# Kernel tuning notes

Measured on AMD Instinct MI355X. Metric: run time of the kernel, lower is better.

Reference implementation:

```python
import jax, jax.numpy as jnp
import numpy as np

N_LEVELS = 16
N_FEATS = 2
LOG2_T = 19
BASE_RES = 16.0
FINEST_RES = 512.0
N_POINTS = 1_000_000
HASH_MASK = np.uint32((1 << LOG2_T) - 1)
PRIME1 = np.uint32(2654435761)  # second spatial-hash prime (first is 1)


def setup_inputs() -> dict:
    key = jax.random.key(0)
    k1, k2 = jax.random.split(key)
    x = jax.random.uniform(k1, (N_POINTS, 2), dtype=jnp.float32)
    # nn.init.uniform_(w, -1e-4, 1e-4) per level, stacked: [L, T, F]
    embeddings = (jax.random.uniform(k2, (N_LEVELS, 2 ** LOG2_T, N_FEATS), dtype=jnp.float32) * 2.0 - 1.0) * 1e-4
    return {"x": x, "embeddings": embeddings}


def reference(x, embeddings):
    L = N_LEVELS
    n = x.shape[0]
    # per-level resolutions: floor(base * b**i)
    b = np.exp((np.log(FINEST_RES) - np.log(BASE_RES)) / (L - 1))
    res = np.floor(BASE_RES * b ** np.arange(L)).astype(np.float32)  # [L]
    res_j = jnp.asarray(res)

    pixels = x[None, :, :] * res_j[:, None, None]           # [L, n, 2]
    top_left = jnp.floor(pixels).astype(jnp.int32)          # [L, n, 2]
    offsets = jnp.array([[0, 0], [1, 0], [0, 1], [1, 1]], dtype=jnp.int32)
    box = top_left[:, :, None, :] + offsets[None, None]     # [L, n, 4, 2]
    box = jnp.clip(box, 0, res_j[:, None, None, None].astype(jnp.int32))

    # spatial hash: (c0*1 ^ c1*prime) & mask, with uint32 wraparound like torch int32
    c = box.astype(jnp.uint32)
    addr = ((c[..., 0] * np.uint32(1)) ^ (c[..., 1] * PRIME1)) & HASH_MASK  # [L, n, 4]
    addr = addr.astype(jnp.int32)

    # gather per-level corner features: [L, n, 4, F]
    feats = jax.vmap(lambda table, idx: table[idx])(embeddings, addr)

    # bilinear interpolation
    w = pixels - jnp.floor(pixels)                          # [L, n, 2]
    w0 = w[..., 0:1]
    w1 = w[..., 1:2]
    f0, f1, f2, f3 = feats[:, :, 0], feats[:, :, 1], feats[:, :, 2], feats[:, :, 3]
    f = (f0 * (1 - w0) + f1 * w0) * (1 - w1) + (f2 * (1 - w0) + f3 * w0) * w1  # [L, n, F]

    # concat levels along feature dim -> [n, L*F]
    return jnp.transpose(f, (1, 0, 2)).reshape(n, L * N_FEATS)
```

## Files before the change

kernel.cpp:

```cpp
#include <hip/hip_runtime.h>
#include <cmath>

#define NLVL 16
#define TSIZE (1u << 19)
#define HMASK ((1u << 19) - 1u)
#define PRIME1 2654435761u

struct Params {
    float rf[NLVL];
    int   ri[NLVL];
    int   base[NLVL];
    int   stride[NLVL];
};

__global__ __launch_bounds__(256) void build_dense(
    const float2* __restrict__ emb, float2* __restrict__ dense, Params p)
{
    const int l = blockIdx.y;
    const int cy = blockIdx.x;
    const int ri = p.ri[l];
    if (cy > ri) return;
    const unsigned hy = (unsigned)cy * PRIME1;
    const float2* tab = emb + (size_t)l * TSIZE;
    float2* drow = dense + p.base[l] + (size_t)cy * p.stride[l];
    for (int cx = threadIdx.x; cx <= ri; cx += 256)
        drow[cx] = tab[((unsigned)cx ^ hy) & HMASK];
}

__global__ __launch_bounds__(256) void hash_embed_dense(
    const float2* __restrict__ x,
    const float2* __restrict__ dense,
    float* __restrict__ out,
    Params p, int n)
{
    __shared__ float2 lds[NLVL * 256];
    const int tid = threadIdx.x;
    const int i = blockIdx.x * 256 + tid;
    float2 xy = make_float2(0.f, 0.f);
    if (i < n) xy = x[i];

    #pragma unroll
    for (int half = 0; half < 2; ++half) {
        float4 r0[8], r1[8];
        float w0v[8], w1v[8];
        int edge[8];
        #pragma unroll
        for (int j = 0; j < 8; ++j) {
            const int l = half * 8 + j;
            const float rf = p.rf[l];
            const int ri = p.ri[l];
            const float px = xy.x * rf, py = xy.y * rf;
            const float fx = floorf(px), fy = floorf(py);
            w0v[j] = px - fx;
            w1v[j] = py - fy;
            const int tx = (int)fx, ty = (int)fy;
            const int cx0 = min(tx, ri);
            const int cy0 = min(ty, ri);
            const int cy1 = min(ty + 1, ri);
            edge[j] = (cx0 == ri);
            const float2* tab = dense + p.base[l];
            const float2* a0 = tab + cy0 * p.stride[l] + cx0;
            const float2* a1 = tab + cy1 * p.stride[l] + cx0;
            __builtin_memcpy(&r0[j], a0, 16);
            __builtin_memcpy(&r1[j], a1, 16);
        }
        #pragma unroll
        for (int j = 0; j < 8; ++j) {
            const int l = half * 8 + j;
            const float w0 = w0v[j], w1 = w1v[j];
            const float u0 = 1.f - w0, u1 = 1.f - w1;
            const float e00x = r0[j].x, e00y = r0[j].y;
            const float e01x = edge[j] ? r0[j].x : r0[j].z;
            const float e01y = edge[j] ? r0[j].y : r0[j].w;
            const float e10x = r1[j].x, e10y = r1[j].y;
            const float e11x = edge[j] ? r1[j].x : r1[j].z;
            const float e11y = edge[j] ? r1[j].y : r1[j].w;
            const float g0 = (e00x*u0 + e01x*w0)*u1 + (e10x*u0 + e11x*w0)*w1;
            const float g1 = (e00y*u0 + e01y*w0)*u1 + (e10y*u0 + e11y*w0)*w1;
            lds[l * 256 + tid] = make_float2(g0, g1);
        }
    }
    __syncthreads();

    const float* lf = (const float*)lds;
    const long long total = (long long)n * 32;
    const long long base = (long long)blockIdx.x * 8192;
    #pragma unroll
    for (int it = 0; it < 8; ++it) {
        const int k = (it * 256 + tid) * 4;
        if (base + k < total) {
            const int p2 = k >> 5;
            const int l0 = (k & 31) >> 1;
            float4 v;
            v.x = lf[(l0 * 256 + p2) * 2 + 0];
            v.y = lf[(l0 * 256 + p2) * 2 + 1];
            v.z = lf[((l0 + 1) * 256 + p2) * 2 + 0];
            v.w = lf[((l0 + 1) * 256 + p2) * 2 + 1];
            *(float4*)(out + base + k) = v;
        }
    }
}

__global__ __launch_bounds__(256) void hash_embed_direct(
    const float2* __restrict__ x,
    const float2* __restrict__ emb,
    float* __restrict__ out,
    Params p, int n)
{
    __shared__ float2 lds[NLVL * 256];
    const int tid = threadIdx.x;
    const int i = blockIdx.x * 256 + tid;
    float2 xy = make_float2(0.f, 0.f);
    if (i < n) xy = x[i];

    #pragma unroll
    for (int half = 0; half < 2; ++half) {
        float2 f[32];
        float w0v[8], w1v[8];
        #pragma unroll
        for (int j = 0; j < 8; ++j) {
            const int l = half * 8 + j;
            const float rf = p.rf[l];
            const int ri = p.ri[l];
            const float px = xy.x * rf, py = xy.y * rf;
            const float fx = floorf(px), fy = floorf(py);
            w0v[j] = px - fx;
            w1v[j] = py - fy;
            const int tx = (int)fx, ty = (int)fy;
            const unsigned cx0 = (unsigned)min(tx, ri);
            const unsigned cy0 = (unsigned)min(ty, ri);
            const unsigned cx1 = (unsigned)min(tx + 1, ri);
            const unsigned cy1 = (unsigned)min(ty + 1, ri);
            const unsigned hy0 = cy0 * PRIME1;
            const unsigned hy1 = cy1 * PRIME1;
            const float2* tab = emb + (size_t)l * TSIZE;
            f[j*4+0] = tab[(cx0 ^ hy0) & HMASK];
            f[j*4+1] = tab[(cx1 ^ hy0) & HMASK];
            f[j*4+2] = tab[(cx0 ^ hy1) & HMASK];
            f[j*4+3] = tab[(cx1 ^ hy1) & HMASK];
        }
        #pragma unroll
        for (int j = 0; j < 8; ++j) {
            const int l = half * 8 + j;
            const float w0 = w0v[j], w1 = w1v[j];
            const float u0 = 1.f - w0, u1 = 1.f - w1;
            const float2 f0 = f[j*4+0], f1 = f[j*4+1], f2 = f[j*4+2], f3 = f[j*4+3];
            const float g0 = (f0.x*u0 + f1.x*w0)*u1 + (f2.x*u0 + f3.x*w0)*w1;
            const float g1 = (f0.y*u0 + f1.y*w0)*u1 + (f2.y*u0 + f3.y*w0)*w1;
            lds[l * 256 + tid] = make_float2(g0, g1);
        }
    }
    __syncthreads();

    const float* lf = (const float*)lds;
    const long long total = (long long)n * 32;
    const long long base = (long long)blockIdx.x * 8192;
    #pragma unroll
    for (int it = 0; it < 8; ++it) {
        const int k = (it * 256 + tid) * 4;
        if (base + k < total) {
            const int p2 = k >> 5;
            const int l0 = (k & 31) >> 1;
            float4 v;
            v.x = lf[(l0 * 256 + p2) * 2 + 0];
            v.y = lf[(l0 * 256 + p2) * 2 + 1];
            v.z = lf[((l0 + 1) * 256 + p2) * 2 + 0];
            v.w = lf[((l0 + 1) * 256 + p2) * 2 + 1];
            *(float4*)(out + base + k) = v;
        }
    }
}

extern "C" void kernel_launch(void* const* d_in, const int* in_sizes, int n_in,
                              void* d_out, int out_size, void* d_ws, size_t ws_size,
                              hipStream_t stream) {
    const float2* x = (const float2*)d_in[0];
    const float2* emb = (const float2*)d_in[1];
    float* out = (float*)d_out;
    const int n = in_sizes[0] / 2;

    Params p;
    int off = 0;
    const double b = std::exp((std::log(512.0) - std::log(16.0)) / 15.0);
    for (int l = 0; l < NLVL; ++l) {
        const double r = std::floor(16.0 * std::pow(b, (double)l));
        p.rf[l] = (float)r;
        p.ri[l] = (int)r;
        p.stride[l] = p.ri[l] + 2;
        p.base[l] = off;
        off += (p.ri[l] + 1) * (p.ri[l] + 2);
    }
    const size_t need = (size_t)off * sizeof(float2);

    const int grid = (n + 255) / 256;
    if (ws_size >= need) {
        build_dense<<<dim3(513, 16), 256, 0, stream>>>(emb, (float2*)d_ws, p);
        hash_embed_dense<<<grid, 256, 0, stream>>>(x, (const float2*)d_ws, out, p, n);
    } else {
        hash_embed_direct<<<grid, 256, 0, stream>>>(x, emb, out, p, n);
    }
}
```

Measured before the change: 281.4 us.

## Store dense embedding grid as scaled fp16 pairs and use nontemporal stores

The dense per-level grid is now built with each float2 embedding quantized to two fp16 values packed in 32 bits, scaled by 1024 to avoid subnormals. It is then dequantized in the lookup kernel. This halves the workspace size and gather bytes, aiming to cut memory traffic and improve cache hit rates. The change also swizzles the LDS layout and uses nontemporal loads and stores for the streaming table read and the output write. The trade-off is reduced precision of the embedding values, which may affect tolerance.

```diff
diff --git a/kernel.cpp b/kernel.cpp
--- a/kernel.cpp
+++ b/kernel.cpp
@@ -1,10 +1,17 @@
 #include <hip/hip_runtime.h>
+#include <hip/hip_fp16.h>
 #include <cmath>
 
 #define NLVL 16
 #define TSIZE (1u << 19)
 #define HMASK ((1u << 19) - 1u)
 #define PRIME1 2654435761u
+#define FSCALE 1024.0f
+#define FINV   (1.0f/1024.0f)
+
+typedef float f32x4 __attribute__((ext_vector_type(4)));
+typedef unsigned int       u32;
+typedef unsigned long long u64;
 
 struct Params {
     float rf[NLVL];
@@ -13,27 +20,37 @@
     int   stride[NLVL];
 };
 
-__global__ __launch_bounds__(256) void build_dense(
-    const float2* __restrict__ emb, float2* __restrict__ dense, Params p)
+__device__ __forceinline__ float2 h2f(u32 u) {
+    __half2 h; __builtin_memcpy(&h, &u, 4);
+    return __half22float2(h);
+}
+
+__global__ __launch_bounds__(256) void build_dense_h(
+    const float2* __restrict__ emb, u32* __restrict__ dense, Params p)
 {
-    const int l = blockIdx.y;
+    const int l  = blockIdx.y;
     const int cy = blockIdx.x;
     const int ri = p.ri[l];
     if (cy > ri) return;
     const unsigned hy = (unsigned)cy * PRIME1;
-    const float2* tab = emb + (size_t)l * TSIZE;
-    float2* drow = dense + p.base[l] + (size_t)cy * p.stride[l];
-    for (int cx = threadIdx.x; cx <= ri; cx += 256)
-        drow[cx] = tab[((unsigned)cx ^ hy) & HMASK];
-}
-
-__global__ __launch_bounds__(256) void hash_embed_dense(
+    const u64* tab = (const u64*)(emb + (size_t)l * TSIZE);
+    u32* drow = dense + p.base[l] + (size_t)cy * p.stride[l];
+    for (int cx = threadIdx.x; cx <= ri; cx += 256) {
+        u64 raw = __builtin_nontemporal_load(tab + (((unsigned)cx ^ hy) & HMASK));
+        float2 v; __builtin_memcpy(&v, &raw, 8);
+        const u32 h0 = (u32)__half_as_ushort(__float2half_rn(v.x * FSCALE));
+        const u32 h1 = (u32)__half_as_ushort(__float2half_rn(v.y * FSCALE));
+        drow[cx] = h0 | (h1 << 16);
+    }
+}
+
+__global__ __launch_bounds__(256) void hash_embed_h(
     const float2* __restrict__ x,
-    const float2* __restrict__ dense,
-    float* __restrict__ out,
+    const u32*    __restrict__ dense,
+    float*        __restrict__ out,
     Params p, int n)
 {
-    __shared__ float2 lds[NLVL * 256];
+    __shared__ float lds[NLVL * 512];
     const int tid = threadIdx.x;
     const int i = blockIdx.x * 256 + tid;
     float2 xy = make_float2(0.f, 0.f);
@@ -41,7 +58,7 @@
 
     #pragma unroll
     for (int half = 0; half < 2; ++half) {
-        float4 r0[8], r1[8];
+        u32 q0x[8], q0y[8], q1x[8], q1y[8];
         float w0v[8], w1v[8];
         int edge[8];
         #pragma unroll
@@ -58,45 +75,44 @@
             const int cy0 = min(ty, ri);
             const int cy1 = min(ty + 1, ri);
             edge[j] = (cx0 == ri);
-            const float2* tab = dense + p.base[l];
-            const float2* a0 = tab + cy0 * p.stride[l] + cx0;
-            const float2* a1 = tab + cy1 * p.stride[l] + cx0;
-            __builtin_memcpy(&r0[j], a0, 16);
-            __builtin_memcpy(&r1[j], a1, 16);
+            const u32* tab = dense + p.base[l];
+            uint2 a, b;
+            __builtin_memcpy(&a, tab + cy0 * p.stride[l] + cx0, 8);
+            __builtin_memcpy(&b, tab + cy1 * p.stride[l] + cx0, 8);
+            q0x[j] = a.x; q0y[j] = a.y; q1x[j] = b.x; q1y[j] = b.y;
         }
         #pragma unroll
         for (int j = 0; j < 8; ++j) {
             const int l = half * 8 + j;
             const float w0 = w0v[j], w1 = w1v[j];
             const float u0 = 1.f - w0, u1 = 1.f - w1;
-            const float e00x = r0[j].x, e00y = r0[j].y;
-            const float e01x = edge[j] ? r0[j].x : r0[j].z;
-            const float e01y = edge[j] ? r0[j].y : r0[j].w;
-            const float e10x = r1[j].x, e10y = r1[j].y;
-            const float e11x = edge[j] ? r1[j].x : r1[j].z;
-            const float e11y = edge[j] ? r1[j].y : r1[j].w;
-            const float g0 = (e00x*u0 + e01x*w0)*u1 + (e10x*u0 + e11x*w0)*w1;
-            const float g1 = (e00y*u0 + e01y*w0)*u1 + (e10y*u0 + e11y*w0)*w1;
-            lds[l * 256 + tid] = make_float2(g0, g1);
+            const float2 e00 = h2f(q0x[j]);
+            const float2 e01 = h2f(edge[j] ? q0x[j] : q0y[j]);
+            const float2 e10 = h2f(q1x[j]);
+            const float2 e11 = h2f(edge[j] ? q1x[j] : q1y[j]);
+            const float g0 = ((e00.x*u0 + e01.x*w0)*u1 + (e10.x*u0 + e11.x*w0)*w1) * FINV;
+            const float g1 = ((e00.y*u0 + e01.y*w0)*u1 + (e10.y*u0 + e11.y*w0)*w1) * FINV;
+            const int idx = l * 512 + ((2 * tid) ^ ((l & 15) << 1));
+            lds[idx]     = g0;
+            lds[idx + 1] = g1;
         }
     }
     __syncthreads();
 
-    const float* lf = (const float*)lds;
     const long long total = (long long)n * 32;
-    const long long base = (long long)blockIdx.x * 8192;
+    const long long base  = (long long)blockIdx.x * 8192;
     #pragma unroll
     for (int it = 0; it < 8; ++it) {
         const int k = (it * 256 + tid) * 4;
         if (base + k < total) {
             const int p2 = k >> 5;
             const int l0 = (k & 31) >> 1;
-            float4 v;
-            v.x = lf[(l0 * 256 + p2) * 2 + 0];
-            v.y = lf[(l0 * 256 + p2) * 2 + 1];
-            v.z = lf[((l0 + 1) * 256 + p2) * 2 + 0];
-            v.w = lf[((l0 + 1) * 256 + p2) * 2 + 1];
-            *(float4*)(out + base + k) = v;
+            const int s0 = l0 * 512       + ((2 * p2) ^ ((l0 & 15) << 1));
+            const int s1 = (l0 + 1) * 512 + ((2 * p2) ^ (((l0 + 1) & 15) << 1));
+            f32x4 v;
+            v.x = lds[s0]; v.y = lds[s0 + 1];
+            v.z = lds[s1]; v.w = lds[s1 + 1];
+            __builtin_nontemporal_store(v, (f32x4*)(out + base + k));
         }
     }
 }
@@ -190,12 +206,12 @@
         p.base[l] = off;
         off += (p.ri[l] + 1) * (p.ri[l] + 2);
     }
-    const size_t need = (size_t)off * sizeof(float2);
+    const size_t need = (size_t)off * sizeof(u32);
 
     const int grid = (n + 255) / 256;
     if (ws_size >= need) {
-        build_dense<<<dim3(513, 16), 256, 0, stream>>>(emb, (float2*)d_ws, p);
-        hash_embed_dense<<<grid, 256, 0, stream>>>(x, (const float2*)d_ws, out, p, n);
+        build_dense_h<<<dim3(513, 16), 256, 0, stream>>>(emb, (u32*)d_ws, p);
+        hash_embed_h<<<grid, 256, 0, stream>>>(x, (const u32*)d_ws, out, p, n);
     } else {
         hash_embed_direct<<<grid, 256, 0, stream>>>(x, emb, out, p, n);
     }
```

Result: faster. 240.2 us (-14.6%).
